# Kernel optimization log

Measured on AMD Instinct MI355X. Metric: run time of the kernel, lower is better.

Reference implementation:

```python
import jax, jax.numpy as jnp
import numpy as np

B, T = 256, 512
V, H, L, O = 29275, 128, 2, 3


def setup_inputs() -> dict:
    key = jax.random.key(0)
    ks = jax.random.split(key, 8)
    s_emb = 1.0  # torch nn.Embedding default init is N(0,1)
    s = 1.0 / np.sqrt(H)  # torch GRU/Linear default U(-1/sqrt(H), 1/sqrt(H))
    return {
        "x": jax.random.randint(ks[0], (B, T), 0, V, dtype=jnp.int32),
        "emb": jax.random.normal(ks[1], (V, H), dtype=jnp.float32) * s_emb,
        "W_ih": jax.random.uniform(ks[2], (L, 3 * H, H), jnp.float32, -s, s),
        "W_hh": jax.random.uniform(ks[3], (L, 3 * H, H), jnp.float32, -s, s),
        "b_ih": jax.random.uniform(ks[4], (L, 3 * H), jnp.float32, -s, s),
        "b_hh": jax.random.uniform(ks[5], (L, 3 * H), jnp.float32, -s, s),
        "fc_w": jax.random.uniform(ks[6], (O, H), jnp.float32, -s, s),
        "fc_b": jax.random.uniform(ks[7], (O,), jnp.float32, -s, s),
    }


def _gru_layer(inp, Wih, Whh, bih, bhh):
    # inp: [B, T, H]. PyTorch GRU gate order: r, z, n.
    gx = jnp.einsum("bth,gh->btg", inp, Wih) + bih  # [B, T, 3H] input-side gates

    def step(h, gx_t):
        gh = h @ Whh.T + bhh  # [B, 3H]
        xr, xz, xn = jnp.split(gx_t, 3, axis=-1)
        hr, hz, hn = jnp.split(gh, 3, axis=-1)
        r = jax.nn.sigmoid(xr + hr)
        z = jax.nn.sigmoid(xz + hz)
        n = jnp.tanh(xn + r * hn)
        h_new = (1.0 - z) * n + z * h
        return h_new, h_new

    h0 = jnp.zeros((inp.shape[0], Whh.shape[1]), dtype=inp.dtype)
    _, outs = jax.lax.scan(step, h0, gx.transpose(1, 0, 2))  # [T, B, H]
    return outs.transpose(1, 0, 2)


def reference(x, emb, W_ih, W_hh, b_ih, b_hh, fc_w, fc_b):
    h = emb[x]  # [B, T, H] embedding lookup
    for l in range(L):  # small fixed layer count; dropout inactive in eval mode
        h = _gru_layer(h, W_ih[l], W_hh[l], b_ih[l], b_hh[l])
    last = jax.nn.relu(h[:, -1])  # [B, H]
    return last @ fc_w.T + fc_b  # [B, O]
```

## Files before the change

### kernel.cpp

```cpp
#include <hip/hip_runtime.h>
#include <hip/hip_bf16.h>

#define B_   256
#define T_   512
#define H_   128
#define G3_  384

#define TM   128
#define TN   128
#define TK   32
#define LDA  132

#define LOG2E_F  1.4426950408889634f
#define LOG2E2_F 2.8853900817779268f

typedef float v4f __attribute__((ext_vector_type(4)));
typedef float v2f __attribute__((ext_vector_type(2)));

__device__ __forceinline__ float fast_rcp(float x) {
    return __builtin_amdgcn_rcpf(x);
}
__device__ __forceinline__ float exp2_raw(float x) {
    return __builtin_amdgcn_exp2f(x);
}

__device__ __forceinline__ void pk_fma(v2f& acc, v2f a, v2f b) {
    asm("v_pk_fma_f32 %0, %1, %2, %0" : "+v"(acc) : "v"(a), "v"(b));
}

__device__ __forceinline__ float bfly_fold4(float v) {
    int x;
    x = __builtin_amdgcn_update_dpp(0, __float_as_int(v), 0x0B1, 0xF, 0xF, true);
    v += __int_as_float(x);
    x = __builtin_amdgcn_update_dpp(0, __float_as_int(v), 0x04E, 0xF, 0xF, true);
    v += __int_as_float(x);
    return v;
}

template<bool GATHER>
__global__ __launch_bounds__(256, 2)
void gx_gemm(const float* __restrict__ X,
             const int*   __restrict__ idx,
             const float* __restrict__ emb,
             const float* __restrict__ W,
             const float* __restrict__ bias,
             const float* __restrict__ bias2,
             float*       __restrict__ gx)
{
    __shared__ __align__(16) float As[2][TK][LDA];
    __shared__ __align__(16) float Bs[2][TK][LDA];

    const int tid = threadIdx.x;
    const int tn  = tid & 15;
    const int tm  = tid >> 4;
    const int n0  = blockIdx.x * TN;
    const int m0  = blockIdx.y * TM;

    const int q  = tid & 7;
    const float* rowA[4];
    const float* rowB[4];
#pragma unroll
    for (int s = 0; s < 4; s++) {
        const int r = (tid >> 3) + 32 * s;
        rowA[s] = GATHER ? (emb + (size_t)idx[m0 + r] * H_)
                         : (X + (size_t)(m0 + r) * H_);
        rowB[s] = W + (size_t)(n0 + r) * H_;
    }

    float4 stA[4], stB[4];
    auto load_chunk = [&](int kc) {
#pragma unroll
        for (int s = 0; s < 4; s++) {
            stA[s] = *(const float4*)(rowA[s] + kc + q * 4);
            stB[s] = *(const float4*)(rowB[s] + kc + q * 4);
        }
    };
    auto store_chunk = [&](int buf) {
#pragma unroll
        for (int s = 0; s < 4; s++) {
            const int r = (tid >> 3) + 32 * s;
#pragma unroll
            for (int d = 0; d < 4; d++) {
                As[buf][q * 4 + d][r] = ((const float*)&stA[s])[d];
                Bs[buf][q * 4 + d][r] = ((const float*)&stB[s])[d];
            }
        }
    };

    float4 acc[2][2][4];
#pragma unroll
    for (int a = 0; a < 2; a++)
#pragma unroll
        for (int b = 0; b < 2; b++)
#pragma unroll
            for (int c = 0; c < 4; c++) acc[a][b][c] = make_float4(0.f, 0.f, 0.f, 0.f);

    load_chunk(0);
    store_chunk(0);
    __syncthreads();

    for (int c = 0; c < 4; c++) {
        if (c < 3) load_chunk((c + 1) * TK);
        const int buf = c & 1;
#pragma unroll 4
        for (int k = 0; k < TK; k++) {
            float4 a0 = *(const float4*)&As[buf][k][tm * 4];
            float4 a1 = *(const float4*)&As[buf][k][64 + tm * 4];
            float4 b0 = *(const float4*)&Bs[buf][k][tn * 4];
            float4 b1 = *(const float4*)&Bs[buf][k][64 + tn * 4];
            float4 av[2] = {a0, a1}, bv[2] = {b0, b1};
#pragma unroll
            for (int mg = 0; mg < 2; mg++)
#pragma unroll
                for (int mi = 0; mi < 4; mi++) {
                    const float am = ((const float*)&av[mg])[mi];
#pragma unroll
                    for (int ng = 0; ng < 2; ng++) {
                        acc[mg][ng][mi].x = fmaf(am, bv[ng].x, acc[mg][ng][mi].x);
                        acc[mg][ng][mi].y = fmaf(am, bv[ng].y, acc[mg][ng][mi].y);
                        acc[mg][ng][mi].z = fmaf(am, bv[ng].z, acc[mg][ng][mi].z);
                        acc[mg][ng][mi].w = fmaf(am, bv[ng].w, acc[mg][ng][mi].w);
                    }
                }
        }
        if (c < 3) {
            store_chunk(buf ^ 1);
            __syncthreads();
        }
    }

    float4 bb0 = *(const float4*)(bias + n0 + tn * 4);
    float4 bb1 = *(const float4*)(bias + n0 + 64 + tn * 4);
    if (n0 < 2 * H_) {
        const float4 c0 = *(const float4*)(bias2 + n0 + tn * 4);
        const float4 c1 = *(const float4*)(bias2 + n0 + 64 + tn * 4);
        bb0.x += c0.x; bb0.y += c0.y; bb0.z += c0.z; bb0.w += c0.w;
        bb1.x += c1.x; bb1.y += c1.y; bb1.z += c1.z; bb1.w += c1.w;
    }
    const float esc = (n0 < 2 * H_) ? LOG2E_F : LOG2E2_F;
#pragma unroll
    for (int mg = 0; mg < 2; mg++)
#pragma unroll
        for (int mi = 0; mi < 4; mi++) {
            const int m = m0 + mg * 64 + tm * 4 + mi;
            float* dst = gx + (size_t)m * G3_ + n0;
            float4 v0 = acc[mg][0][mi];
            v0.x = (v0.x + bb0.x) * esc; v0.y = (v0.y + bb0.y) * esc;
            v0.z = (v0.z + bb0.z) * esc; v0.w = (v0.w + bb0.w) * esc;
            float4 v1 = acc[mg][1][mi];
            v1.x = (v1.x + bb1.x) * esc; v1.y = (v1.y + bb1.y) * esc;
            v1.z = (v1.z + bb1.z) * esc; v1.w = (v1.w + bb1.w) * esc;
            *(float4*)(dst + tn * 4) = v0;
            *(float4*)(dst + 64 + tn * 4) = v1;
        }
}

template<bool STORE_H, bool FINAL>
__global__ __launch_bounds__(512)
__attribute__((amdgpu_waves_per_eu(2, 2)))
void gru_rec(const float* __restrict__ gx,
             const float* __restrict__ Whh,
             const float* __restrict__ bhh,
             float*       __restrict__ hseq,
             const float* __restrict__ fc_w,
             const float* __restrict__ fc_b,
             float*       __restrict__ out)
{
    __shared__ __align__(16) float h2[2][H_];

    const int tid = threadIdx.x;
    const int b   = blockIdx.x;
    const int jg  = tid >> 2;
    const int ks  = tid & 3;

    v2f Wr[16], Wz[16], Wn[16];
    {
        const v4f* wr = (const v4f*)(Whh + (size_t)(jg      ) * H_ + ks * 32);
        const v4f* wz = (const v4f*)(Whh + (size_t)(jg + 128) * H_ + ks * 32);
        const v4f* wn = (const v4f*)(Whh + (size_t)(jg + 256) * H_ + ks * 32);
#pragma unroll
        for (int c = 0; c < 8; c++) {
            v4f t;
            t = wr[c] * LOG2E_F;  Wr[2 * c] = t.lo; Wr[2 * c + 1] = t.hi;
            t = wz[c] * LOG2E_F;  Wz[2 * c] = t.lo; Wz[2 * c + 1] = t.hi;
            t = wn[c] * LOG2E2_F; Wn[2 * c] = t.lo; Wn[2 * c + 1] = t.hi;
        }
    }

    const float bhn = bhh[jg + 2 * H_] * LOG2E2_F;

    const float* gxb = gx + (size_t)b * T_ * G3_;
    float gr = gxb[jg], gz = gxb[jg + 128], gn = gxb[jg + 256];
    float h_old = 0.0f;

    if (tid < H_) h2[0][tid] = 0.0f;

    const int hw = ((jg >> 2) & 7) * 16 + (jg >> 5) * 4 + (jg & 3);
    const int hb = ks * 4;

    const float* gnx = gxb + G3_;
    float* hp = STORE_H ? (hseq + (size_t)b * T_ * H_ + jg) : nullptr;

    __syncthreads();

#define GRU_STEP(HIN, HOUT)                                                   \
    {                                                                         \
        const float gr2_ = gnx[jg];                                           \
        const float gz2_ = gnx[jg + 128];                                     \
        const float gn2_ = gnx[jg + 256];                                     \
        gnx += G3_;                                                           \
        v2f pr = {0.f, 0.f}, pz = {0.f, 0.f}, pn = {0.f, 0.f};                \
        _Pragma("unroll")                                                     \
        for (int c = 0; c < 8; c++) {                                         \
            v4f hv = *(const v4f*)&(HIN)[16 * c + hb];                        \
            v2f hlo = hv.lo, hhi = hv.hi;                                     \
            pk_fma(pr, hlo, Wr[2 * c]);  pk_fma(pr, hhi, Wr[2 * c + 1]);      \
            pk_fma(pz, hlo, Wz[2 * c]);  pk_fma(pz, hhi, Wz[2 * c + 1]);      \
            pk_fma(pn, hlo, Wn[2 * c]);  pk_fma(pn, hhi, Wn[2 * c + 1]);      \
        }                                                                     \
        const float p0 = bfly_fold4(pr.x + pr.y);                             \
        const float p1 = bfly_fold4(pz.x + pz.y);                             \
        const float p2 = bfly_fold4(pn.x + pn.y);                             \
        const float r_ = fast_rcp(1.0f + exp2_raw(-(gr + p0)));               \
        const float z_ = fast_rcp(1.0f + exp2_raw(-(gz + p1)));               \
        const float n_ = fmaf(-2.0f,                                          \
            fast_rcp(exp2_raw(gn + r_ * (p2 + bhn)) + 1.0f), 1.0f);           \
        h_old = fmaf(z_, h_old - n_, n_);                                     \
        if (ks == 0) {                                                        \
            (HOUT)[hw] = h_old;                                               \
            if (STORE_H) *hp = h_old;                                         \
        }                                                                     \
        if (STORE_H) hp += H_;                                                \
        gr = gr2_; gz = gz2_; gn = gn2_;                                      \
        __syncthreads();                                                      \
    }

    for (int t = 0; t < T_; t += 2) {
        GRU_STEP(h2[0], h2[1])
        GRU_STEP(h2[1], h2[0])
    }
#undef GRU_STEP

    if (FINAL) {
        if (ks == 0) h2[1][jg] = fmaxf(h_old, 0.0f);
        __syncthreads();
        if (tid < 3) {
            float acc = fc_b[tid];
            const float* fw = fc_w + tid * H_;
#pragma unroll
            for (int k = 0; k < H_; k++) acc = fmaf(h2[1][k], fw[k], acc);
            out[b * 3 + tid] = acc;
        }
    }
}

extern "C" void kernel_launch(void* const* d_in, const int* in_sizes, int n_in,
                              void* d_out, int out_size, void* d_ws, size_t ws_size,
                              hipStream_t stream)
{
    const int*   x    = (const int*)  d_in[0];
    const float* emb  = (const float*)d_in[1];
    const float* W_ih = (const float*)d_in[2];
    const float* W_hh = (const float*)d_in[3];
    const float* b_ih = (const float*)d_in[4];
    const float* b_hh = (const float*)d_in[5];
    const float* fc_w = (const float*)d_in[6];
    const float* fc_b = (const float*)d_in[7];
    float* out = (float*)d_out;

    const int M = B_ * T_;
    const size_t gx_f32 = (size_t)M * G3_ * sizeof(float);

    float* gx = (float*)d_ws;
    float* h1 = (float*)((char*)d_ws + gx_f32);

    dim3 ggx(G3_ / TN, M / TM);
    dim3 bgx(256);
    dim3 grec(B_), brec(512);

    hipLaunchKernelGGL((gx_gemm<true>), ggx, bgx, 0, stream,
                       nullptr, x, emb, W_ih, b_ih, b_hh, gx);
    hipLaunchKernelGGL((gru_rec<true, false>), grec, brec, 0, stream,
                       gx, W_hh, b_hh, h1, nullptr, nullptr, nullptr);
    hipLaunchKernelGGL((gx_gemm<false>), ggx, bgx, 0, stream,
                       h1, nullptr, nullptr, W_ih + G3_ * H_, b_ih + G3_,
                       b_hh + G3_, gx);
    hipLaunchKernelGGL((gru_rec<false, true>), grec, brec, 0, stream,
                       gx, W_hh + G3_ * H_, b_hh + G3_, nullptr, fc_w, fc_b, out);
}
```

Baseline: 826.3 us.

## Split first-layer GRU recurrence dot products eight ways across 1024 threads

Adds a gru_rec8 kernel in which each hidden unit's three recurrent dot products are split over 8 lanes instead of 4, using 1024-thread blocks and a three-stage DPP butterfly reduction. Each thread now holds half as many W_hh weights in registers and does half the FMAs per timestep. The aim is to shorten the latency of each serial timestep in the first layer. The cost is an extra cross-lane reduction stage and a larger block to synchronise at every step. The second layer still runs the original 512-thread kernel.

```diff
diff --git a/kernel.cpp b/kernel.cpp
--- a/kernel.cpp
+++ b/kernel.cpp
@@ -33,6 +33,17 @@
     x = __builtin_amdgcn_update_dpp(0, __float_as_int(v), 0x0B1, 0xF, 0xF, true);
     v += __int_as_float(x);
     x = __builtin_amdgcn_update_dpp(0, __float_as_int(v), 0x04E, 0xF, 0xF, true);
+    v += __int_as_float(x);
+    return v;
+}
+
+__device__ __forceinline__ float bfly_fold8(float v) {
+    int x;
+    x = __builtin_amdgcn_update_dpp(0, __float_as_int(v), 0x0B1, 0xF, 0xF, true);
+    v += __int_as_float(x);
+    x = __builtin_amdgcn_update_dpp(0, __float_as_int(v), 0x04E, 0xF, 0xF, true);
+    v += __int_as_float(x);
+    x = __builtin_amdgcn_update_dpp(0, __float_as_int(v), 0x141, 0xF, 0xF, true);
     v += __int_as_float(x);
     return v;
 }
@@ -153,6 +164,122 @@
             *(float4*)(dst + tn * 4) = v0;
             *(float4*)(dst + 64 + tn * 4) = v1;
         }
+}
+
+template<bool STORE_H, bool FINAL>
+__global__ __launch_bounds__(1024)
+__attribute__((amdgpu_waves_per_eu(4, 4)))
+void gru_rec8(const float* __restrict__ gx,
+              const float* __restrict__ Whh,
+              const float* __restrict__ bhh,
+              float*       __restrict__ hseq,
+              const float* __restrict__ fc_w,
+              const float* __restrict__ fc_b,
+              float*       __restrict__ out)
+{
+    __shared__ __align__(16) float h2[2][H_];
+
+    const int tid = threadIdx.x;
+    const int b   = blockIdx.x;
+    const int jg  = tid >> 3;
+    const int ks  = tid & 7;
+
+    v2f Wr[8], Wz[8], Wn[8];
+    {
+        const float* r0 = Whh + (size_t)(jg      ) * H_ + ks * 16;
+        const float* z0 = Whh + (size_t)(jg + 128) * H_ + ks * 16;
+        const float* n0 = Whh + (size_t)(jg + 256) * H_ + ks * 16;
+#pragma unroll
+        for (int c = 0; c < 4; c++) {
+            const int f = ((c + ks) & 3) * 4;
+            v4f t;
+            t = *(const v4f*)(r0 + f) * LOG2E_F;
+            Wr[2 * c] = t.lo; Wr[2 * c + 1] = t.hi;
+            t = *(const v4f*)(z0 + f) * LOG2E_F;
+            Wz[2 * c] = t.lo; Wz[2 * c + 1] = t.hi;
+            t = *(const v4f*)(n0 + f) * LOG2E2_F;
+            Wn[2 * c] = t.lo; Wn[2 * c + 1] = t.hi;
+        }
+    }
+
+    const float bhn = bhh[jg + 2 * H_] * LOG2E2_F;
+
+    const float* gxb = gx + (size_t)b * T_ * G3_;
+    float gr = gxb[jg], gz = gxb[jg + H_], gn = gxb[jg + 2 * H_];
+    float h_old = 0.0f;
+
+    if (tid < H_) h2[0][tid] = 0.0f;
+
+    const int ho0 = ks * 16 + (((0 + ks) & 3) << 2);
+    const int ho1 = ks * 16 + (((1 + ks) & 3) << 2);
+    const int ho2 = ks * 16 + (((2 + ks) & 3) << 2);
+    const int ho3 = ks * 16 + (((3 + ks) & 3) << 2);
+
+    const float* gnx = gxb + G3_;
+    float* hp = STORE_H ? (hseq + (size_t)b * T_ * H_ + jg) : nullptr;
+
+    __syncthreads();
+
+#define GRU_STEP8(HIN, HOUT)                                                  \
+    {                                                                         \
+        const float gr2_ = gnx[jg];                                           \
+        const float gz2_ = gnx[jg + H_];                                      \
+        const float gn2_ = gnx[jg + 2 * H_];                                  \
+        gnx += G3_;                                                           \
+        v2f pr = {0.f, 0.f}, pz = {0.f, 0.f}, pn = {0.f, 0.f};                \
+        {                                                                     \
+            v4f hv;                                                           \
+            hv = *(const v4f*)&(HIN)[ho0];                                    \
+            pk_fma(pr, hv.lo, Wr[0]);  pk_fma(pr, hv.hi, Wr[1]);              \
+            pk_fma(pz, hv.lo, Wz[0]);  pk_fma(pz, hv.hi, Wz[1]);              \
+            pk_fma(pn, hv.lo, Wn[0]);  pk_fma(pn, hv.hi, Wn[1]);              \
+            hv = *(const v4f*)&(HIN)[ho1];                                    \
+            pk_fma(pr, hv.lo, Wr[2]);  pk_fma(pr, hv.hi, Wr[3]);              \
+            pk_fma(pz, hv.lo, Wz[2]);  pk_fma(pz, hv.hi, Wz[3]);              \
+            pk_fma(pn, hv.lo, Wn[2]);  pk_fma(pn, hv.hi, Wn[3]);              \
+            hv = *(const v4f*)&(HIN)[ho2];                                    \
+            pk_fma(pr, hv.lo, Wr[4]);  pk_fma(pr, hv.hi, Wr[5]);              \
+            pk_fma(pz, hv.lo, Wz[4]);  pk_fma(pz, hv.hi, Wz[5]);              \
+            pk_fma(pn, hv.lo, Wn[4]);  pk_fma(pn, hv.hi, Wn[5]);              \
+            hv = *(const v4f*)&(HIN)[ho3];                                    \
+            pk_fma(pr, hv.lo, Wr[6]);  pk_fma(pr, hv.hi, Wr[7]);              \
+            pk_fma(pz, hv.lo, Wz[6]);  pk_fma(pz, hv.hi, Wz[7]);              \
+            pk_fma(pn, hv.lo, Wn[6]);  pk_fma(pn, hv.hi, Wn[7]);              \
+        }                                                                     \
+        const float p0 = bfly_fold8(pr.x + pr.y);                             \
+        const float p1 = bfly_fold8(pz.x + pz.y);                             \
+        const float p2 = bfly_fold8(pn.x + pn.y);                             \
+        const float r_ = fast_rcp(1.0f + exp2_raw(-(gr + p0)));               \
+        const float z_ = fast_rcp(1.0f + exp2_raw(-(gz + p1)));               \
+        const float n_ = fmaf(-2.0f,                                          \
+            fast_rcp(exp2_raw(gn + r_ * (p2 + bhn)) + 1.0f), 1.0f);           \
+        h_old = fmaf(z_, h_old - n_, n_);                                     \
+        if (ks == 0) {                                                        \
+            (HOUT)[jg] = h_old;                                               \
+            if (STORE_H) *hp = h_old;                                         \
+        }                                                                     \
+        if (STORE_H) hp += H_;                                                \
+        gr = gr2_; gz = gz2_; gn = gn2_;                                      \
+        __syncthreads();                                                      \
+    }
+
+    for (int t = 0; t < T_; t += 2) {
+        GRU_STEP8(h2[0], h2[1])
+        GRU_STEP8(h2[1], h2[0])
+    }
+#undef GRU_STEP8
+
+    if (FINAL) {
+        if (ks == 0) h2[1][jg] = fmaxf(h_old, 0.0f);
+        __syncthreads();
+        if (tid < 3) {
+            float acc = fc_b[tid];
+            const float* fw = fc_w + tid * H_;
+#pragma unroll
+            for (int k = 0; k < H_; k++) acc = fmaf(h2[1][k], fw[k], acc);
+            out[b * 3 + tid] = acc;
+        }
+    }
 }
 
 template<bool STORE_H, bool FINAL>
@@ -276,15 +403,15 @@
 
     dim3 ggx(G3_ / TN, M / TM);
     dim3 bgx(256);
-    dim3 grec(B_), brec(512);
+    dim3 grec(B_);
 
     hipLaunchKernelGGL((gx_gemm<true>), ggx, bgx, 0, stream,
                        nullptr, x, emb, W_ih, b_ih, b_hh, gx);
-    hipLaunchKernelGGL((gru_rec<true, false>), grec, brec, 0, stream,
+    hipLaunchKernelGGL((gru_rec8<true, false>), grec, dim3(1024), 0, stream,
                        gx, W_hh, b_hh, h1, nullptr, nullptr, nullptr);
     hipLaunchKernelGGL((gx_gemm<false>), ggx, bgx, 0, stream,
                        h1, nullptr, nullptr, W_ih + G3_ * H_, b_ih + G3_,
                        b_hh + G3_, gx);
-    hipLaunchKernelGGL((gru_rec<false, true>), grec, brec, 0, stream,
+    hipLaunchKernelGGL((gru_rec<false, true>), grec, dim3(512), 0, stream,
                        gx, W_hh + G3_ * H_, b_hh + G3_, nullptr, fc_w, fc_b, out);
 }
```

Result: slower. 911.6 us (+10.3%).

## Repartition layer-1 GRU recurrence: 2 hidden units per 8-lane group

Applied to the files above, without the earlier changes.

Adds a new recurrence kernel for the first GRU layer. Each 8-thread group now computes two hidden units, with each lane covering a 16-wide K slice. The weights are held in registers, the dot products use packed FMAs, and partial sums are reduced with an 8-lane DPP butterfly. Reads of the shared hidden state are rotated per lane to spread LDS accesses. The goal is to reuse each shared-memory h load across two output units and shorten the per-step reduction, at the cost of more weight registers per thread. Only layer 1 uses the new kernel; layer 2 keeps the old one.

```diff
diff --git a/kernel.cpp b/kernel.cpp
--- a/kernel.cpp
+++ b/kernel.cpp
@@ -33,6 +33,17 @@
     x = __builtin_amdgcn_update_dpp(0, __float_as_int(v), 0x0B1, 0xF, 0xF, true);
     v += __int_as_float(x);
     x = __builtin_amdgcn_update_dpp(0, __float_as_int(v), 0x04E, 0xF, 0xF, true);
+    v += __int_as_float(x);
+    return v;
+}
+
+__device__ __forceinline__ float bfly_fold8(float v) {
+    int x;
+    x = __builtin_amdgcn_update_dpp(0, __float_as_int(v), 0x0B1, 0xF, 0xF, true);
+    v += __int_as_float(x);
+    x = __builtin_amdgcn_update_dpp(0, __float_as_int(v), 0x04E, 0xF, 0xF, true);
+    v += __int_as_float(x);
+    x = __builtin_amdgcn_update_dpp(0, __float_as_int(v), 0x141, 0xF, 0xF, true);
     v += __int_as_float(x);
     return v;
 }
@@ -153,6 +164,158 @@
             *(float4*)(dst + tn * 4) = v0;
             *(float4*)(dst + 64 + tn * 4) = v1;
         }
+}
+
+template<bool STORE_H, bool FINAL>
+__global__ __launch_bounds__(512)
+__attribute__((amdgpu_waves_per_eu(2, 2)))
+void gru_recB(const float* __restrict__ gx,
+              const float* __restrict__ Whh,
+              const float* __restrict__ bhh,
+              float*       __restrict__ hseq,
+              const float* __restrict__ fc_w,
+              const float* __restrict__ fc_b,
+              float*       __restrict__ out)
+{
+    __shared__ __align__(16) float h2[2][H_];
+
+    const int tid = threadIdx.x;
+    const int b   = blockIdx.x;
+    const int jg2 = tid >> 3;
+    const int ks  = tid & 7;
+    const int j0  = jg2 * 2;
+    const int rot = ks >> 1;
+
+    v2f W0r[8], W0z[8], W0n[8], W1r[8], W1z[8], W1n[8];
+    {
+        const float* r0 = Whh + (size_t)(j0      ) * H_ + ks * 16;
+        const float* z0 = Whh + (size_t)(j0 + 128) * H_ + ks * 16;
+        const float* n0 = Whh + (size_t)(j0 + 256) * H_ + ks * 16;
+#pragma unroll
+        for (int c = 0; c < 4; c++) {
+            const int f = ((c + rot) & 3) * 4;
+            v4f t;
+            t = *(const v4f*)(r0 + f) * LOG2E_F;
+            W0r[2 * c] = t.lo; W0r[2 * c + 1] = t.hi;
+            t = *(const v4f*)(r0 + H_ + f) * LOG2E_F;
+            W1r[2 * c] = t.lo; W1r[2 * c + 1] = t.hi;
+            t = *(const v4f*)(z0 + f) * LOG2E_F;
+            W0z[2 * c] = t.lo; W0z[2 * c + 1] = t.hi;
+            t = *(const v4f*)(z0 + H_ + f) * LOG2E_F;
+            W1z[2 * c] = t.lo; W1z[2 * c + 1] = t.hi;
+            t = *(const v4f*)(n0 + f) * LOG2E2_F;
+            W0n[2 * c] = t.lo; W0n[2 * c + 1] = t.hi;
+            t = *(const v4f*)(n0 + H_ + f) * LOG2E2_F;
+            W1n[2 * c] = t.lo; W1n[2 * c + 1] = t.hi;
+        }
+    }
+
+    float2 bhn2 = *(const float2*)(bhh + j0 + 2 * H_);
+    bhn2.x *= LOG2E2_F; bhn2.y *= LOG2E2_F;
+
+    const float* gxb = gx + (size_t)b * T_ * G3_;
+    const float* gp  = gxb + j0;
+    float2 gr = *(const float2*)(gp);
+    float2 gz = *(const float2*)(gp + H_);
+    float2 gn = *(const float2*)(gp + 2 * H_);
+    gp += G3_;
+    float2 h_old; h_old.x = 0.0f; h_old.y = 0.0f;
+
+    if (tid < H_) h2[0][tid] = 0.0f;
+
+    const int ho0 = ks * 16 + (((0 + rot) & 3) << 2);
+    const int ho1 = ks * 16 + (((1 + rot) & 3) << 2);
+    const int ho2 = ks * 16 + (((2 + rot) & 3) << 2);
+    const int ho3 = ks * 16 + (((3 + rot) & 3) << 2);
+
+    float* hp = STORE_H ? (hseq + (size_t)b * T_ * H_ + j0) : nullptr;
+
+    __syncthreads();
+
+#define GRU_STEPB(HIN, HOUT)                                                  \
+    {                                                                         \
+        const float2 gr2_ = *(const float2*)(gp);                             \
+        const float2 gz2_ = *(const float2*)(gp + H_);                        \
+        const float2 gn2_ = *(const float2*)(gp + 2 * H_);                    \
+        gp += G3_;                                                            \
+        v2f p0r = {0.f, 0.f}, p0z = {0.f, 0.f}, p0n = {0.f, 0.f};             \
+        v2f p1r = {0.f, 0.f}, p1z = {0.f, 0.f}, p1n = {0.f, 0.f};             \
+        {                                                                     \
+            v4f hv; v2f hlo, hhi;                                             \
+            hv = *(const v4f*)&(HIN)[ho0]; hlo = hv.lo; hhi = hv.hi;          \
+            pk_fma(p0r, hlo, W0r[0]); pk_fma(p0r, hhi, W0r[1]);               \
+            pk_fma(p0z, hlo, W0z[0]); pk_fma(p0z, hhi, W0z[1]);               \
+            pk_fma(p0n, hlo, W0n[0]); pk_fma(p0n, hhi, W0n[1]);               \
+            pk_fma(p1r, hlo, W1r[0]); pk_fma(p1r, hhi, W1r[1]);               \
+            pk_fma(p1z, hlo, W1z[0]); pk_fma(p1z, hhi, W1z[1]);               \
+            pk_fma(p1n, hlo, W1n[0]); pk_fma(p1n, hhi, W1n[1]);               \
+            hv = *(const v4f*)&(HIN)[ho1]; hlo = hv.lo; hhi = hv.hi;          \
+            pk_fma(p0r, hlo, W0r[2]); pk_fma(p0r, hhi, W0r[3]);               \
+            pk_fma(p0z, hlo, W0z[2]); pk_fma(p0z, hhi, W0z[3]);               \
+            pk_fma(p0n, hlo, W0n[2]); pk_fma(p0n, hhi, W0n[3]);               \
+            pk_fma(p1r, hlo, W1r[2]); pk_fma(p1r, hhi, W1r[3]);               \
+            pk_fma(p1z, hlo, W1z[2]); pk_fma(p1z, hhi, W1z[3]);               \
+            pk_fma(p1n, hlo, W1n[2]); pk_fma(p1n, hhi, W1n[3]);               \
+            hv = *(const v4f*)&(HIN)[ho2]; hlo = hv.lo; hhi = hv.hi;          \
+            pk_fma(p0r, hlo, W0r[4]); pk_fma(p0r, hhi, W0r[5]);               \
+            pk_fma(p0z, hlo, W0z[4]); pk_fma(p0z, hhi, W0z[5]);               \
+            pk_fma(p0n, hlo, W0n[4]); pk_fma(p0n, hhi, W0n[5]);               \
+            pk_fma(p1r, hlo, W1r[4]); pk_fma(p1r, hhi, W1r[5]);               \
+            pk_fma(p1z, hlo, W1z[4]); pk_fma(p1z, hhi, W1z[5]);               \
+            pk_fma(p1n, hlo, W1n[4]); pk_fma(p1n, hhi, W1n[5]);               \
+            hv = *(const v4f*)&(HIN)[ho3]; hlo = hv.lo; hhi = hv.hi;          \
+            pk_fma(p0r, hlo, W0r[6]); pk_fma(p0r, hhi, W0r[7]);               \
+            pk_fma(p0z, hlo, W0z[6]); pk_fma(p0z, hhi, W0z[7]);               \
+            pk_fma(p0n, hlo, W0n[6]); pk_fma(p0n, hhi, W0n[7]);               \
+            pk_fma(p1r, hlo, W1r[6]); pk_fma(p1r, hhi, W1r[7]);               \
+            pk_fma(p1z, hlo, W1z[6]); pk_fma(p1z, hhi, W1z[7]);               \
+            pk_fma(p1n, hlo, W1n[6]); pk_fma(p1n, hhi, W1n[7]);               \
+        }                                                                     \
+        const float s0r = bfly_fold8(p0r.x + p0r.y);                          \
+        const float s0z = bfly_fold8(p0z.x + p0z.y);                          \
+        const float s0n = bfly_fold8(p0n.x + p0n.y);                          \
+        const float s1r = bfly_fold8(p1r.x + p1r.y);                          \
+        const float s1z = bfly_fold8(p1z.x + p1z.y);                          \
+        const float s1n = bfly_fold8(p1n.x + p1n.y);                          \
+        const float r0_ = fast_rcp(1.0f + exp2_raw(-(gr.x + s0r)));           \
+        const float z0_ = fast_rcp(1.0f + exp2_raw(-(gz.x + s0z)));           \
+        const float n0_ = fmaf(-2.0f,                                         \
+            fast_rcp(exp2_raw(gn.x + r0_ * (s0n + bhn2.x)) + 1.0f), 1.0f);    \
+        h_old.x = fmaf(z0_, h_old.x - n0_, n0_);                              \
+        const float r1_ = fast_rcp(1.0f + exp2_raw(-(gr.y + s1r)));           \
+        const float z1_ = fast_rcp(1.0f + exp2_raw(-(gz.y + s1z)));           \
+        const float n1_ = fmaf(-2.0f,                                         \
+            fast_rcp(exp2_raw(gn.y + r1_ * (s1n + bhn2.y)) + 1.0f), 1.0f);    \
+        h_old.y = fmaf(z1_, h_old.y - n1_, n1_);                              \
+        if (ks == 0) {                                                        \
+            *(float2*)&(HOUT)[j0] = h_old;                                    \
+            if (STORE_H) *(float2*)hp = h_old;                                \
+        }                                                                     \
+        if (STORE_H) hp += H_;                                                \
+        gr = gr2_; gz = gz2_; gn = gn2_;                                      \
+        __syncthreads();                                                      \
+    }
+
+    for (int t = 0; t < T_; t += 2) {
+        GRU_STEPB(h2[0], h2[1])
+        GRU_STEPB(h2[1], h2[0])
+    }
+#undef GRU_STEPB
+
+    if (FINAL) {
+        if (ks == 0) {
+            h2[1][j0]     = fmaxf(h_old.x, 0.0f);
+            h2[1][j0 + 1] = fmaxf(h_old.y, 0.0f);
+        }
+        __syncthreads();
+        if (tid < 3) {
+            float acc = fc_b[tid];
+            const float* fw = fc_w + tid * H_;
+#pragma unroll
+            for (int k = 0; k < H_; k++) acc = fmaf(h2[1][k], fw[k], acc);
+            out[b * 3 + tid] = acc;
+        }
+    }
 }
 
 template<bool STORE_H, bool FINAL>
@@ -280,7 +443,7 @@
 
     hipLaunchKernelGGL((gx_gemm<true>), ggx, bgx, 0, stream,
                        nullptr, x, emb, W_ih, b_ih, b_hh, gx);
-    hipLaunchKernelGGL((gru_rec<true, false>), grec, brec, 0, stream,
+    hipLaunchKernelGGL((gru_recB<true, false>), grec, brec, 0, stream,
                        gx, W_hh, b_hh, h1, nullptr, nullptr, nullptr);
     hipLaunchKernelGGL((gx_gemm<false>), ggx, bgx, 0, stream,
                        h1, nullptr, nullptr, W_ih + G3_ * H_, b_ih + G3_,
```

New measurement: 959.2 us. 1.16x slower.
